# Kernel tuning notes

Hardware: AMD Instinct MI355X
Metric: run time of the kernel (lower is better)

The kernel has to match this reference:

```python
import jax, jax.numpy as jnp
import numpy as np

B, L, D, H, NB = 8, 256, 128, 4, 2
HD = D // H
N_ITEMS, TIME_SPAN = 50000, 256
EPS = 1e-8
NEG = -(2.0 ** 32) + 1.0  # torch uses -2**32+1 padding value


def _ln(x, g, b):
    m = jnp.mean(x, -1, keepdims=True)
    v = jnp.mean((x - m) ** 2, -1, keepdims=True)
    return (x - m) / jnp.sqrt(v + EPS) * g + b


def setup_inputs() -> dict:
    ks = iter(jax.random.split(jax.random.key(0), 40))

    def nrm(shape, s=0.02):
        return jax.random.normal(next(ks), shape, jnp.float32) * s

    inp = {
        "user_ids": jax.random.randint(next(ks), (B,), 0, 1000),
        "log_seqs": jax.random.randint(next(ks), (B, L), 0, N_ITEMS + 1),
        "time_matrices": jax.random.randint(next(ks), (B, L, L), 0, TIME_SPAN + 1),
        "pos_seqs": jax.random.randint(next(ks), (B, L), 1, N_ITEMS + 1),
        "neg_seqs": jax.random.randint(next(ks), (B, L), 1, N_ITEMS + 1),
    }
    inp["item_emb"] = nrm((N_ITEMS + 1, D)).at[0].set(0.0)  # padding_idx=0
    inp["posK_emb"] = nrm((L, D))
    inp["posV_emb"] = nrm((L, D))
    inp["timeK_emb"] = nrm((TIME_SPAN + 1, D))
    inp["timeV_emb"] = nrm((TIME_SPAN + 1, D))
    inp["ln1_g"] = jnp.ones((NB, D)); inp["ln1_b"] = jnp.zeros((NB, D))
    inp["Wq"] = nrm((NB, D, D)); inp["bq"] = jnp.zeros((NB, D))
    inp["Wk"] = nrm((NB, D, D)); inp["bk"] = jnp.zeros((NB, D))
    inp["Wv"] = nrm((NB, D, D)); inp["bv"] = jnp.zeros((NB, D))
    inp["ln2_g"] = jnp.ones((NB, D)); inp["ln2_b"] = jnp.zeros((NB, D))
    inp["W1"] = nrm((NB, D, D)); inp["b1"] = jnp.zeros((NB, D))
    inp["W2"] = nrm((NB, D, D)); inp["b2"] = jnp.zeros((NB, D))
    inp["lnf_g"] = jnp.ones((D,)); inp["lnf_b"] = jnp.zeros((D,))
    return inp


def reference(user_ids, log_seqs, time_matrices, pos_seqs, neg_seqs,
              item_emb, posK_emb, posV_emb, timeK_emb, timeV_emb,
              ln1_g, ln1_b, Wq, bq, Wk, bk, Wv, bv, ln2_g, ln2_b,
              W1, b1, W2, b2, lnf_g, lnf_b):
    # dropout layers are identity in eval mode
    seqs = item_emb[log_seqs] * jnp.sqrt(jnp.float32(D))          # [B,L,D]
    tK = timeK_emb[time_matrices].reshape(B, L, L, H, HD)          # [B,Lq,Lk,H,hd]
    tV = timeV_emb[time_matrices].reshape(B, L, L, H, HD)
    pad = log_seqs == 0                                            # [B,L]
    seqs = seqs * (~pad)[..., None]
    causal = jnp.triu(jnp.ones((L, L), bool), 1)                   # ~tril -> masked
    # time_mask masks by QUERY position (matches torch unsqueeze(-1).expand)
    mask = pad[:, None, :, None] | causal[None, None]              # [B,1,Lq,Lk]
    posKh = posK_emb.reshape(L, H, HD)
    posVh = posV_emb.reshape(L, H, HD)
    for i in range(NB):
        q_in = _ln(seqs, ln1_g[i], ln1_b[i])
        Qh = (q_in @ Wq[i] + bq[i]).reshape(B, L, H, HD).transpose(0, 2, 1, 3)
        Kh = (seqs @ Wk[i] + bk[i]).reshape(B, L, H, HD).transpose(0, 2, 1, 3)
        Vh = (seqs @ Wv[i] + bv[i]).reshape(B, L, H, HD).transpose(0, 2, 1, 3)
        scores = jnp.einsum("bhqd,bhkd->bhqk", Qh, Kh)
        scores = scores + jnp.einsum("bhqd,khd->bhqk", Qh, posKh)
        scores = scores + jnp.einsum("bqkhd,bhqd->bhqk", tK, Qh)
        scores = scores / jnp.sqrt(jnp.float32(HD))
        scores = jnp.where(mask, NEG, scores)
        A = jax.nn.softmax(scores, axis=-1)                        # [B,H,Lq,Lk]
        out = jnp.einsum("bhqk,bhkd->bhqd", A, Vh)
        out = out + jnp.einsum("bhqk,khd->bhqd", A, posVh)
        out = out + jnp.einsum("bhqk,bqkhd->bhqd", A, tV)
        out = out.transpose(0, 2, 1, 3).reshape(B, L, D)
        seqs = q_in + out                                          # residual on Q
        seqs = _ln(seqs, ln2_g[i], ln2_b[i])
        h = jax.nn.relu(seqs @ W1[i] + b1[i])                      # conv1d k=1 == linear
        seqs = seqs + (h @ W2[i] + b2[i])
        seqs = seqs * (~pad)[..., None]
    feats = _ln(seqs, lnf_g, lnf_b)
    pos_logits = jnp.sum(feats * item_emb[pos_seqs], -1)           # [B,L]
    neg_logits = jnp.sum(feats * item_emb[neg_seqs], -1)
    return (pos_logits, neg_logits)
```

## Files before the change

### kernel.cpp

```cpp
#include <hip/hip_runtime.h>
#include <hip/hip_bf16.h>

#define L_ 256
#define H_ 4
#define ROWS 2048
#define NEGV (-4294967295.0f)

typedef unsigned short us16;

__device__ __forceinline__ float us2f(us16 u){ return __uint_as_float(((unsigned)u)<<16); }
__device__ __forceinline__ us16 f2us(float f){ __hip_bfloat16 h=__float2bfloat16(f); return *(us16*)&h; }

__device__ __forceinline__ float dot2bf(unsigned x, unsigned y, float c){
#if __has_builtin(__builtin_amdgcn_fdot2_f32_bf16)
    typedef __bf16 bf2 __attribute__((ext_vector_type(2)));
    union U{ unsigned u; bf2 v; };
    U ux, uy; ux.u=x; uy.u=y;
    return __builtin_amdgcn_fdot2_f32_bf16(ux.v, uy.v, c, false);
#else
    float r=fmaf(us2f((us16)(x&0xffffu)), us2f((us16)(y&0xffffu)), c);
    return fmaf(us2f((us16)(x>>16)), us2f((us16)(y>>16)), r);
#endif
}

struct KArgs {
    const int *log_seqs, *tmat, *pos_seqs, *neg_seqs;
    const float *item_emb, *posK, *posV, *timeK, *timeV;
    const float *ln1g, *ln1b, *bq, *bk, *bv, *ln2g, *ln2b, *b1, *b2, *lnfg, *lnfb;
    const float *Wq, *Wk, *Wv, *W1, *W2;
    float *qin0, *qin1, *out;
    unsigned *wsP;
    us16 *tmK, *tmV, *Qb0, *Kb0, *Vb0, *Qb1, *Kb1, *Vb1;
};

struct __align__(16) Smem {
    float    sS[8*256];
    float    sPjPr[2056];
    int      sTM[512];
    unsigned sQb[128];
    float    sX[256];
    unsigned sXb[128];
    unsigned sHb[128];
    unsigned sYb[128];
    float    sRed[4], sRed2[4], sRB[8];
};

__device__ __forceinline__ float gemv128(const unsigned* __restrict__ wp,
                                         const unsigned* __restrict__ xp, int c){
    float s0=0.f, s1=0.f;
    #pragma unroll 8
    for(int kp=0;kp<64;kp+=2){
        s0=dot2bf(xp[kp],   wp[kp*128+c],     s0);
        s1=dot2bf(xp[kp+1], wp[(kp+1)*128+c], s1);
    }
    return s0+s1;
}

__device__ __forceinline__ void ln_rows(float* sA,
        const float* __restrict__ g, const float* __restrict__ b,
        float* qin_out, int r0, int tid){
    int r=tid>>5, l=tid&31;
    float* x=sA+r*128;
    float x0=x[l],x1=x[l+32],x2=x[l+64],x3=x[l+96];
    float s=x0+x1+x2+x3;
    #pragma unroll
    for(int o=16;o;o>>=1) s+=__shfl_xor(s,o,64);
    float m=s*(1.f/128.f);
    float d0=x0-m,d1=x1-m,d2=x2-m,d3=x3-m;
    float v=d0*d0+d1*d1+d2*d2+d3*d3;
    #pragma unroll
    for(int o=16;o;o>>=1) v+=__shfl_xor(v,o,64);
    float rstd=rsqrtf(v*(1.f/128.f)+1e-8f);
    float y0=d0*rstd*g[l]+b[l];
    float y1=d1*rstd*g[l+32]+b[l+32];
    float y2=d2*rstd*g[l+64]+b[l+64];
    float y3=d3*rstd*g[l+96]+b[l+96];
    x[l]=y0; x[l+32]=y1; x[l+64]=y2; x[l+96]=y3;
    if(qin_out){
        float* q=qin_out+(size_t)(r0+r)*128;
        q[l]=y0; q[l+32]=y1; q[l+64]=y2; q[l+96]=y3;
    }
}

__global__ __launch_bounds__(256) void k_pre(KArgs a){
    __shared__ __align__(16) float sA[1024];
    int tid=threadIdx.x, bid=blockIdx.x;
    if(bid<768){
        int m=bid>>8, rg=bid&255, r0=rg*8;
        {
            int rl=tid>>5, c4=tid&31;
            int id=a.log_seqs[r0+rl];
            float4 v=((const float4*)a.item_emb)[id*32+c4];
            float sc = id? 11.3137085f : 0.f;
            v.x*=sc; v.y*=sc; v.z*=sc; v.w*=sc;
            ((float4*)sA)[tid]=v;
        }
        __syncthreads();
        if(m==0){ ln_rows(sA, a.ln1g, a.ln1b, a.qin0, r0, tid); __syncthreads(); }
        const float* Wsrc=(m==0)?a.Wq:(m==1)?a.Wk:a.Wv;
        int cp=tid&63, rp=tid>>6, c0=2*cp, ra=2*rp, rb=ra+1;
        float a00=0,a01=0,a10=0,a11=0;
        const float* Ar=sA+ra*128;
        const float* Br=sA+rb*128;
        #pragma unroll 8
        for(int kk=0;kk<128;kk++){
            float2 wp=((const float2*)(Wsrc+(size_t)kk*128))[cp];
            float x0=Ar[kk], x1=Br[kk];
            a00=fmaf(x0,wp.x,a00); a01=fmaf(x0,wp.y,a01);
            a10=fmaf(x1,wp.x,a10); a11=fmaf(x1,wp.y,a11);
        }
        int r_a=r0+ra, r_b=r0+rb;
        if(m==0){
            float b0v=a.bq[c0], b1v=a.bq[c0+1];
            ushort2 s0; s0.x=f2us(a00+b0v); s0.y=f2us(a01+b1v);
            ushort2 s1; s1.x=f2us(a10+b0v); s1.y=f2us(a11+b1v);
            *(ushort2*)(a.Qb0+(size_t)r_a*128+c0)=s0;
            *(ushort2*)(a.Qb0+(size_t)r_b*128+c0)=s1;
        } else if(m==1){
            float b0v=a.bk[c0], b1v=a.bk[c0+1];
            int qa=r_a&255, qb2=r_b&255;
            ushort2 s0; s0.x=f2us(a00+b0v+a.posK[qa*128+c0]);  s0.y=f2us(a01+b1v+a.posK[qa*128+c0+1]);
            ushort2 s1; s1.x=f2us(a10+b0v+a.posK[qb2*128+c0]); s1.y=f2us(a11+b1v+a.posK[qb2*128+c0+1]);
            *(ushort2*)(a.Kb0+(size_t)r_a*128+c0)=s0;
            *(ushort2*)(a.Kb0+(size_t)r_b*128+c0)=s1;
        } else {
            float b0v=a.bv[c0], b1v=a.bv[c0+1];
            int qa=r_a&255, qb2=r_b&255;
            unsigned lo0=f2us(a00+b0v+a.posV[qa*128+c0]);
            unsigned lo1=f2us(a01+b1v+a.posV[qa*128+c0+1]);
            unsigned hi0=f2us(a10+b0v+a.posV[qb2*128+c0]);
            unsigned hi1=f2us(a11+b1v+a.posV[qb2*128+c0+1]);
            unsigned* Vo=(unsigned*)a.Vb0+((size_t)r_a>>1)*128;
            Vo[c0]  =lo0|(hi0<<16);
            Vo[c0+1]=lo1|(hi1<<16);
        }
    } else if(bid<880){
        int j=bid-768; int m=j>>4; int sub=j&15;
        const float* base;
        switch(m){
            case 0: base=a.W1; break;        case 1: base=a.W2; break;
            case 2: base=a.Wq+16384; break;  case 3: base=a.Wk+16384; break;
            case 4: base=a.Wv+16384; break;  case 5: base=a.W1+16384; break;
            default: base=a.W2+16384; break;
        }
        unsigned* dst=a.wsP+(size_t)m*8192;
        #pragma unroll
        for(int t2=0;t2<2;t2++){
            int o=sub*512+t2*256+tid;
            int kp=o>>7, c=o&127;
            unsigned lo=f2us(base[(size_t)(2*kp)*128+c]);
            unsigned hi=f2us(base[(size_t)(2*kp+1)*128+c]);
            dst[o]=lo|(hi<<16);
        }
    } else {
        int gi=(bid-880)*256+tid;
        if(gi<8224){
            float4 v=((const float4*)a.timeK)[gi];
            ushort4 o; o.x=f2us(v.x);o.y=f2us(v.y);o.z=f2us(v.z);o.w=f2us(v.w);
            ((ushort4*)a.tmK)[gi]=o;
        } else if(gi<16448){
            int g2=gi-8224;
            float4 v=((const float4*)a.timeV)[g2];
            ushort4 o; o.x=f2us(v.x);o.y=f2us(v.y);o.z=f2us(v.z);o.w=f2us(v.w);
            ((ushort4*)a.tmV)[g2]=o;
        }
    }
}

__global__ __launch_bounds__(256,7) void k_blk(KArgs a, int layer){
    __shared__ Smem sm;
    float* sPj=sm.sPjPr;
    float* sPr=sm.sPjPr;
    int tid=threadIdx.x, bid=blockIdx.x;
    int b=bid>>7, p=bid&127;
    int q1=p, q2=255-p, b0=b*L_;
    int r1=b0+q1, r2=b0+q2;
    bool pad1=a.log_seqs[r1]==0, pad2=a.log_seqs[r2]==0;
    const us16* Qb = layer? a.Qb1:a.Qb0;
    const us16* Kb = layer? a.Kb1:a.Kb0;
    const unsigned* Vbu = (const unsigned*)(layer? a.Vb1:a.Vb0);
    const float* qin = layer? a.qin1:a.qin0;
    const float scale=0.17677669529663687f;

    if(tid<128){
        int rowq=tid>>6, j=tid&63;
        int r=rowq?r2:r1;
        sm.sQb[rowq*64+j]=((const unsigned*)Qb)[(size_t)r*64+j];
    }
    sm.sTM[tid]    =a.tmat[(size_t)r1*L_+tid];
    sm.sTM[256+tid]=a.tmat[(size_t)r2*L_+tid];
    __syncthreads();

    {
        int ch=tid&15, h=ch>>2;
        uint4 qv0=((const uint4*)(sm.sQb))[ch];
        uint4 qv1=((const uint4*)(sm.sQb+64))[ch];
        for(int t=tid>>4; t<257; t+=16){
            uint4 tv=((const uint4*)(a.tmK+(size_t)t*128))[ch];
            float p0=0.f,p1=0.f;
            p0=dot2bf(qv0.x,tv.x,p0); p0=dot2bf(qv0.y,tv.y,p0);
            p0=dot2bf(qv0.z,tv.z,p0); p0=dot2bf(qv0.w,tv.w,p0);
            p1=dot2bf(qv1.x,tv.x,p1); p1=dot2bf(qv1.y,tv.y,p1);
            p1=dot2bf(qv1.z,tv.z,p1); p1=dot2bf(qv1.w,tv.w,p1);
            p0+=__shfl_xor(p0,1,64); p0+=__shfl_xor(p0,2,64);
            p1+=__shfl_xor(p1,1,64); p1+=__shfl_xor(p1,2,64);
            if((ch&3)==0){
                sPj[t*4+h]       =p0;
                sPj[1028+t*4+h]  =p1;
            }
        }
    }

    {
        int ch=tid&15, g=tid>>4, h=ch>>2;
        uint4 qv0=((const uint4*)(sm.sQb))[ch];
        uint4 qv1=((const uint4*)(sm.sQb+64))[ch];
        #pragma unroll
        for(int pass=0;pass<16;pass++){
            int k=pass*16+g;
            uint4 kv=((const uint4*)(Kb+(size_t)(b0+k)*128))[ch];
            float p0=0.f,p1=0.f;
            p0=dot2bf(qv0.x,kv.x,p0); p0=dot2bf(qv0.y,kv.y,p0);
            p0=dot2bf(qv0.z,kv.z,p0); p0=dot2bf(qv0.w,kv.w,p0);
            p1=dot2bf(qv1.x,kv.x,p1); p1=dot2bf(qv1.y,kv.y,p1);
            p1=dot2bf(qv1.z,kv.z,p1); p1=dot2bf(qv1.w,kv.w,p1);
            p0+=__shfl_xor(p0,1,64); p0+=__shfl_xor(p0,2,64);
            p1+=__shfl_xor(p1,1,64); p1+=__shfl_xor(p1,2,64);
            if((ch&3)==0){
                sm.sS[h*256+k]    =p0;
                sm.sS[(4+h)*256+k]=p1;
            }
        }
    }
    __syncthreads();

    {
        int h=tid>>6, lane=tid&63;
        #pragma unroll
        for(int i2=0;i2<2;i2++){
            int qq=i2?q2:q1; bool pad=i2?pad2:pad1;
            float* row=sm.sS+(i2*4+h)*256;
            const int*   tmr=sm.sTM+i2*256;
            const float* pjb=sPj+i2*1028;
            int k0=lane, k1=lane+64, k2=lane+128, k3=lane+192;
            float v0=(k0<=qq&&!pad)? (row[k0]+pjb[tmr[k0]*4+h])*scale : NEGV;
            float v1=(k1<=qq&&!pad)? (row[k1]+pjb[tmr[k1]*4+h])*scale : NEGV;
            float v2=(k2<=qq&&!pad)? (row[k2]+pjb[tmr[k2]*4+h])*scale : NEGV;
            float v3=(k3<=qq&&!pad)? (row[k3]+pjb[tmr[k3]*4+h])*scale : NEGV;
            float mm=fmaxf(fmaxf(v0,v1),fmaxf(v2,v3));
            #pragma unroll
            for(int o=32;o;o>>=1) mm=fmaxf(mm,__shfl_xor(mm,o,64));
            float e0=__expf(v0-mm),e1=__expf(v1-mm),e2=__expf(v2-mm),e3=__expf(v3-mm);
            float ss=e0+e1+e2+e3;
            #pragma unroll
            for(int o=32;o;o>>=1) ss+=__shfl_xor(ss,o,64);
            float inv=1.f/ss;
            us16* ar=(us16*)row;
            ar[lane]    =f2us(e0*inv); ar[lane+64] =f2us(e1*inv);
            ar[lane+128]=f2us(e2*inv); ar[lane+192]=f2us(e3*inv);
        }
    }
    __syncthreads();

    {
        int i2=tid>>7, s8=(tid>>4)&7, dq=tid&15;
        int qq=i2?q2:q1; bool pad=i2?pad2:pad1;
        int kend=pad?L_:qq+1;
        int k0=s8*32;
        int kmax=kend-k0; kmax=kmax<0?0:(kmax>32?32:kmax);
        int npair=(kmax+1)>>1;
        const unsigned* arow=(const unsigned*)(sm.sS+(i2*4+(dq>>2))*256);
        const int* tmrow=sm.sTM+i2*256;
        float ac0=0,ac1=0,ac2=0,ac3=0,ac4=0,ac5=0,ac6=0,ac7=0;
        for(int kp=0;kp<npair;kp++){
            int kx=k0+2*kp;
            unsigned aa=arow[kx>>1];
            int tma=tmrow[kx], tmb=tmrow[kx+1];
            const uint4* Vp=(const uint4*)(Vbu+((size_t)(b0+kx)>>1)*128+dq*8);
            uint4 va=Vp[0], vb4=Vp[1];
            uint4 ta=((const uint4*)(a.tmV+(size_t)tma*128))[dq];
            uint4 tb=((const uint4*)(a.tmV+(size_t)tmb*128))[dq];
            ac0=dot2bf(aa,va.x,ac0);  ac1=dot2bf(aa,va.y,ac1);
            ac2=dot2bf(aa,va.z,ac2);  ac3=dot2bf(aa,va.w,ac3);
            ac4=dot2bf(aa,vb4.x,ac4); ac5=dot2bf(aa,vb4.y,ac5);
            ac6=dot2bf(aa,vb4.z,ac6); ac7=dot2bf(aa,vb4.w,ac7);
            unsigned p0=__builtin_amdgcn_perm(tb.x,ta.x,0x05040100u);
            unsigned p1=__builtin_amdgcn_perm(tb.x,ta.x,0x07060302u);
            unsigned p2=__builtin_amdgcn_perm(tb.y,ta.y,0x05040100u);
            unsigned p3=__builtin_amdgcn_perm(tb.y,ta.y,0x07060302u);
            unsigned p4=__builtin_amdgcn_perm(tb.z,ta.z,0x05040100u);
            unsigned p5=__builtin_amdgcn_perm(tb.z,ta.z,0x07060302u);
            unsigned p6=__builtin_amdgcn_perm(tb.w,ta.w,0x05040100u);
            unsigned p7=__builtin_amdgcn_perm(tb.w,ta.w,0x07060302u);
            ac0=dot2bf(aa,p0,ac0); ac1=dot2bf(aa,p1,ac1);
            ac2=dot2bf(aa,p2,ac2); ac3=dot2bf(aa,p3,ac3);
            ac4=dot2bf(aa,p4,ac4); ac5=dot2bf(aa,p5,ac5);
            ac6=dot2bf(aa,p6,ac6); ac7=dot2bf(aa,p7,ac7);
        }
        float* dst=sPr+(i2*8+s8)*128+dq*8;
        ((float4*)dst)[0]=make_float4(ac0,ac1,ac2,ac3);
        ((float4*)dst)[1]=make_float4(ac4,ac5,ac6,ac7);
    }
    __syncthreads();

    int ii=tid>>7, l=tid&127;
    bool padown = ii? pad2:pad1;
    int rr = ii? r2:r1;
    int qown = ii? q2:q1;
    {
        float v=qin[(size_t)rr*128+l];
        #pragma unroll
        for(int sl=0;sl<8;sl++) v+=sPr[(ii*8+sl)*128+l];
        float s=v, s2=v*v;
        #pragma unroll
        for(int o=32;o;o>>=1){ s+=__shfl_xor(s,o,64); s2+=__shfl_xor(s2,o,64); }
        if((tid&63)==0){ sm.sRed[ii*2+((tid>>6)&1)]=s; sm.sRed2[ii*2+((tid>>6)&1)]=s2; }
        __syncthreads();
        float m =(sm.sRed[ii*2] +sm.sRed[ii*2+1]) *(1.f/128.f);
        float ms=(sm.sRed2[ii*2]+sm.sRed2[ii*2+1])*(1.f/128.f);
        float rstd=rsqrtf(fmaxf(ms-m*m,0.f)+1e-8f);
        float y=(v-m)*rstd*a.ln2g[layer*128+l]+a.ln2b[layer*128+l];
        sm.sX[ii*128+l]=y;
        ((us16*)sm.sXb)[ii*128+l]=f2us(y);
    }
    __syncthreads();

    int cc=l;
    {
        float h1=gemv128(a.wsP+(size_t)(layer?5:0)*8192, sm.sXb+ii*64, cc);
        h1=fmaxf(h1+a.b1[layer*128+cc],0.f);
        ((us16*)sm.sHb)[ii*128+cc]=f2us(h1);
    }
    __syncthreads();
    float f;
    {
        f=gemv128(a.wsP+(size_t)(layer?6:1)*8192, sm.sHb+ii*64, cc)
          +a.b2[layer*128+cc]+sm.sX[ii*128+cc];
        if(padown) f=0.f;
    }

    if(layer==0){
        ((us16*)sm.sYb)[ii*128+cc]=f2us(f);
        float s=f, s2=f*f;
        #pragma unroll
        for(int o=32;o;o>>=1){ s+=__shfl_xor(s,o,64); s2+=__shfl_xor(s2,o,64); }
        if((tid&63)==0){ sm.sRB[ii*2+((tid>>6)&1)]=s; sm.sRB[4+ii*2+((tid>>6)&1)]=s2; }
        __syncthreads();
        float m =(sm.sRB[ii*2]  +sm.sRB[ii*2+1]) *(1.f/128.f);
        float ms=(sm.sRB[4+ii*2]+sm.sRB[5+ii*2])*(1.f/128.f);
        float rstd=rsqrtf(fmaxf(ms-m*m,0.f)+1e-8f);
        float y1=(f-m)*rstd*a.ln1g[128+cc]+a.ln1b[128+cc];
        a.qin1[(size_t)rr*128+cc]=y1;
        ((us16*)sm.sXb)[ii*128+cc]=f2us(y1);
        __syncthreads();
        float accq=gemv128(a.wsP+(size_t)2*8192, sm.sXb+ii*64, cc)+a.bq[128+cc];
        a.Qb1[(size_t)rr*128+cc]=f2us(accq);
        float acck=gemv128(a.wsP+(size_t)3*8192, sm.sYb+ii*64, cc)+a.bk[128+cc]+a.posK[qown*128+cc];
        a.Kb1[(size_t)rr*128+cc]=f2us(acck);
        float accv=gemv128(a.wsP+(size_t)4*8192, sm.sYb+ii*64, cc)+a.bv[128+cc]+a.posV[qown*128+cc];
        ((us16*)a.Vb1)[((size_t)rr>>1)*256+2*cc+(rr&1)]=f2us(accv);
    } else {
        float s=f, s2=f*f;
        #pragma unroll
        for(int o=32;o;o>>=1){ s+=__shfl_xor(s,o,64); s2+=__shfl_xor(s2,o,64); }
        if((tid&63)==0){ sm.sRB[ii*2+((tid>>6)&1)]=s; sm.sRB[4+ii*2+((tid>>6)&1)]=s2; }
        __syncthreads();
        float m =(sm.sRB[ii*2]  +sm.sRB[ii*2+1]) *(1.f/128.f);
        float ms=(sm.sRB[4+ii*2]+sm.sRB[5+ii*2])*(1.f/128.f);
        float rstd=rsqrtf(fmaxf(ms-m*m,0.f)+1e-8f);
        sm.sX[ii*128+cc]=(f-m)*rstd*a.lnfg[cc]+a.lnfb[cc];
        __syncthreads();
        int w=tid>>6, lane=tid&63;
        int rowi=w>>1, neg=w&1;
        int rg = rowi? r2:r1;
        int id = neg? a.neg_seqs[rg] : a.pos_seqs[rg];
        const float* e=a.item_emb+(size_t)id*128;
        float s2l = sm.sX[rowi*128+lane]*e[lane] + sm.sX[rowi*128+lane+64]*e[lane+64];
        #pragma unroll
        for(int o=32;o;o>>=1) s2l+=__shfl_xor(s2l,o,64);
        if(lane==0) a.out[neg*ROWS+rg]=s2l;
    }
}

extern "C" void kernel_launch(void* const* d_in, const int* in_sizes, int n_in,
                              void* d_out, int out_size, void* d_ws, size_t ws_size,
                              hipStream_t stream) {
    KArgs a;
    a.log_seqs=(const int*)d_in[1];
    a.tmat    =(const int*)d_in[2];
    a.pos_seqs=(const int*)d_in[3];
    a.neg_seqs=(const int*)d_in[4];
    a.item_emb=(const float*)d_in[5];
    a.posK =(const float*)d_in[6];
    a.posV =(const float*)d_in[7];
    a.timeK=(const float*)d_in[8];
    a.timeV=(const float*)d_in[9];
    a.ln1g=(const float*)d_in[10];
    a.ln1b=(const float*)d_in[11];
    a.Wq=(const float*)d_in[12];
    a.bq=(const float*)d_in[13];
    a.Wk=(const float*)d_in[14];
    a.bk=(const float*)d_in[15];
    a.Wv=(const float*)d_in[16];
    a.bv=(const float*)d_in[17];
    a.ln2g=(const float*)d_in[18];
    a.ln2b=(const float*)d_in[19];
    a.W1=(const float*)d_in[20];
    a.b1=(const float*)d_in[21];
    a.W2=(const float*)d_in[22];
    a.b2=(const float*)d_in[23];
    a.lnfg=(const float*)d_in[24];
    a.lnfb=(const float*)d_in[25];

    const size_t MB=1u<<20;
    char* w=(char*)d_ws;
    a.qin0=(float*)(w+0*MB);
    a.qin1=(float*)(w+1*MB);
    a.Qb0 =(us16*) (w+2*MB);
    a.Kb0 =(us16*) (w+2*MB+512*1024);
    a.Vb0 =(us16*) (w+3*MB);
    a.Qb1 =(us16*) (w+3*MB+512*1024);
    a.Kb1 =(us16*) (w+4*MB);
    a.Vb1 =(us16*) (w+4*MB+512*1024);
    a.wsP =(unsigned*)(w+5*MB);
    a.tmK =(us16*) (w+5*MB+256*1024);
    a.tmV =(us16*) (w+5*MB+384*1024);
    a.out =(float*)d_out;

    k_pre<<<946,256,0,stream>>>(a);
    k_blk<<<1024,256,0,stream>>>(a,0);
    k_blk<<<1024,256,0,stream>>>(a,1);
}
```

Before: 192.7 us.

## Split attention and FFN/projection tail into separate kernels with 4 rows per block

The fused per-layer kernel is split in two. The attention kernel now ends after LN2 and writes its output to a new global buffer. A separate tail kernel then runs the FFN, LN and next-layer QKV projections (or the final logits), with each block handling 4 rows so every weight load from global memory feeds two rows' dot products. This halves weight traffic per row and frees shared memory in the attention kernel, at the cost of two extra launches and an extra global round-trip for the activations.

New measurement: 205.4 us. +6.6%, slower.

```diff
diff --git a/kernel.cpp b/kernel.cpp
--- a/kernel.cpp
+++ b/kernel.cpp
@@ -28,33 +28,18 @@
     const float *item_emb, *posK, *posV, *timeK, *timeV;
     const float *ln1g, *ln1b, *bq, *bk, *bv, *ln2g, *ln2b, *b1, *b2, *lnfg, *lnfb;
     const float *Wq, *Wk, *Wv, *W1, *W2;
-    float *qin0, *qin1, *out;
+    float *qin0, *qin1, *xo0, *xo1, *out;
     unsigned *wsP;
     us16 *tmK, *tmV, *Qb0, *Kb0, *Vb0, *Qb1, *Kb1, *Vb1;
 };
 
-struct __align__(16) Smem {
+struct __align__(16) SmemA {
     float    sS[8*256];
     float    sPjPr[2056];
     int      sTM[512];
     unsigned sQb[128];
-    float    sX[256];
-    unsigned sXb[128];
-    unsigned sHb[128];
-    unsigned sYb[128];
-    float    sRed[4], sRed2[4], sRB[8];
+    float    sRed[4], sRed2[4];
 };
-
-__device__ __forceinline__ float gemv128(const unsigned* __restrict__ wp,
-                                         const unsigned* __restrict__ xp, int c){
-    float s0=0.f, s1=0.f;
-    #pragma unroll 8
-    for(int kp=0;kp<64;kp+=2){
-        s0=dot2bf(xp[kp],   wp[kp*128+c],     s0);
-        s1=dot2bf(xp[kp+1], wp[(kp+1)*128+c], s1);
-    }
-    return s0+s1;
-}
 
 __device__ __forceinline__ void ln_rows(float* sA,
         const float* __restrict__ g, const float* __restrict__ b,
@@ -167,8 +152,8 @@
     }
 }
 
-__global__ __launch_bounds__(256,7) void k_blk(KArgs a, int layer){
-    __shared__ Smem sm;
+__global__ __launch_bounds__(256,7) void k_attn(KArgs a, int layer){
+    __shared__ SmemA sm;
     float* sPj=sm.sPjPr;
     float* sPr=sm.sPjPr;
     int tid=threadIdx.x, bid=blockIdx.x;
@@ -180,6 +165,7 @@
     const us16* Kb = layer? a.Kb1:a.Kb0;
     const unsigned* Vbu = (const unsigned*)(layer? a.Vb1:a.Vb0);
     const float* qin = layer? a.qin1:a.qin0;
+    float* xo = layer? a.xo1 : a.xo0;
     const float scale=0.17677669529663687f;
 
     if(tid<128){
@@ -304,9 +290,7 @@
     __syncthreads();
 
     int ii=tid>>7, l=tid&127;
-    bool padown = ii? pad2:pad1;
     int rr = ii? r2:r1;
-    int qown = ii? q2:q1;
     {
         float v=qin[(size_t)rr*128+l];
         #pragma unroll
@@ -320,65 +304,161 @@
         float ms=(sm.sRed2[ii*2]+sm.sRed2[ii*2+1])*(1.f/128.f);
         float rstd=rsqrtf(fmaxf(ms-m*m,0.f)+1e-8f);
         float y=(v-m)*rstd*a.ln2g[layer*128+l]+a.ln2b[layer*128+l];
-        sm.sX[ii*128+l]=y;
-        ((us16*)sm.sXb)[ii*128+l]=f2us(y);
+        xo[(size_t)rr*128+l]=y;
+    }
+}
+
+__global__ __launch_bounds__(256,8) void k_tail(KArgs a, int layer){
+    __shared__ __align__(16) float    xf[4*128];
+    __shared__ __align__(16) unsigned xb[4*64];
+    __shared__ __align__(16) unsigned hb[4*64];
+    __shared__ __align__(16) unsigned yb[4*64];
+    __shared__ float sR[16];
+    int tid=threadIdx.x, bid=blockIdx.x;
+    int c=tid&127, ii=tid>>7, wh=(tid>>6)&1;
+    int base=bid*4;
+    int ra=base+ii, rb=base+2+ii;
+    bool padA=a.log_seqs[ra]==0, padB=a.log_seqs[rb]==0;
+    const float* xo = layer? a.xo1 : a.xo0;
+    for(int j=tid;j<512;j+=256){
+        float v=xo[(size_t)base*128+j];
+        xf[j]=v;
+        ((us16*)xb)[j]=f2us(v);
     }
     __syncthreads();
 
-    int cc=l;
-    {
-        float h1=gemv128(a.wsP+(size_t)(layer?5:0)*8192, sm.sXb+ii*64, cc);
-        h1=fmaxf(h1+a.b1[layer*128+cc],0.f);
-        ((us16*)sm.sHb)[ii*128+cc]=f2us(h1);
+    {
+        const unsigned* wp=a.wsP+(size_t)(layer?5:0)*8192;
+        float s0=0.f,s1=0.f;
+        #pragma unroll 8
+        for(int kp=0;kp<64;kp++){
+            unsigned w=wp[kp*128+c];
+            s0=dot2bf(xb[ii*64+kp],     w, s0);
+            s1=dot2bf(xb[(ii+2)*64+kp], w, s1);
+        }
+        float b1v=a.b1[layer*128+c];
+        ((us16*)hb)[ii*128+c]    =f2us(fmaxf(s0+b1v,0.f));
+        ((us16*)hb)[(ii+2)*128+c]=f2us(fmaxf(s1+b1v,0.f));
     }
     __syncthreads();
-    float f;
-    {
-        f=gemv128(a.wsP+(size_t)(layer?6:1)*8192, sm.sHb+ii*64, cc)
-          +a.b2[layer*128+cc]+sm.sX[ii*128+cc];
-        if(padown) f=0.f;
+
+    float f0,f1;
+    {
+        const unsigned* wp=a.wsP+(size_t)(layer?6:1)*8192;
+        float s0=0.f,s1=0.f;
+        #pragma unroll 8
+        for(int kp=0;kp<64;kp++){
+            unsigned w=wp[kp*128+c];
+            s0=dot2bf(hb[ii*64+kp],     w, s0);
+            s1=dot2bf(hb[(ii+2)*64+kp], w, s1);
+        }
+        float b2v=a.b2[layer*128+c];
+        f0=s0+b2v+xf[ii*128+c];     if(padA) f0=0.f;
+        f1=s1+b2v+xf[(ii+2)*128+c]; if(padB) f1=0.f;
     }
 
     if(layer==0){
-        ((us16*)sm.sYb)[ii*128+cc]=f2us(f);
-        float s=f, s2=f*f;
-        #pragma unroll
-        for(int o=32;o;o>>=1){ s+=__shfl_xor(s,o,64); s2+=__shfl_xor(s2,o,64); }
-        if((tid&63)==0){ sm.sRB[ii*2+((tid>>6)&1)]=s; sm.sRB[4+ii*2+((tid>>6)&1)]=s2; }
+        ((us16*)yb)[ii*128+c]    =f2us(f0);
+        ((us16*)yb)[(ii+2)*128+c]=f2us(f1);
+        float s0=f0,q0=f0*f0,s1=f1,q1=f1*f1;
+        #pragma unroll
+        for(int o=32;o;o>>=1){
+            s0+=__shfl_xor(s0,o,64); q0+=__shfl_xor(q0,o,64);
+            s1+=__shfl_xor(s1,o,64); q1+=__shfl_xor(q1,o,64);
+        }
+        if((tid&63)==0){
+            sR[ii*8+wh*4+0]=s0; sR[ii*8+wh*4+1]=q0;
+            sR[ii*8+wh*4+2]=s1; sR[ii*8+wh*4+3]=q1;
+        }
         __syncthreads();
-        float m =(sm.sRB[ii*2]  +sm.sRB[ii*2+1]) *(1.f/128.f);
-        float ms=(sm.sRB[4+ii*2]+sm.sRB[5+ii*2])*(1.f/128.f);
-        float rstd=rsqrtf(fmaxf(ms-m*m,0.f)+1e-8f);
-        float y1=(f-m)*rstd*a.ln1g[128+cc]+a.ln1b[128+cc];
-        a.qin1[(size_t)rr*128+cc]=y1;
-        ((us16*)sm.sXb)[ii*128+cc]=f2us(y1);
+        float m0=(sR[ii*8+0]+sR[ii*8+4])*(1.f/128.f);
+        float e0=(sR[ii*8+1]+sR[ii*8+5])*(1.f/128.f);
+        float m1=(sR[ii*8+2]+sR[ii*8+6])*(1.f/128.f);
+        float e1=(sR[ii*8+3]+sR[ii*8+7])*(1.f/128.f);
+        float r0=rsqrtf(fmaxf(e0-m0*m0,0.f)+1e-8f);
+        float r1=rsqrtf(fmaxf(e1-m1*m1,0.f)+1e-8f);
+        float g=a.ln1g[128+c], bb=a.ln1b[128+c];
+        float y0=(f0-m0)*r0*g+bb;
+        float y1=(f1-m1)*r1*g+bb;
+        a.qin1[(size_t)ra*128+c]=y0;
+        a.qin1[(size_t)rb*128+c]=y1;
+        ((us16*)xb)[ii*128+c]    =f2us(y0);
+        ((us16*)xb)[(ii+2)*128+c]=f2us(y1);
         __syncthreads();
-        float accq=gemv128(a.wsP+(size_t)2*8192, sm.sXb+ii*64, cc)+a.bq[128+cc];
-        a.Qb1[(size_t)rr*128+cc]=f2us(accq);
-        float acck=gemv128(a.wsP+(size_t)3*8192, sm.sYb+ii*64, cc)+a.bk[128+cc]+a.posK[qown*128+cc];
-        a.Kb1[(size_t)rr*128+cc]=f2us(acck);
-        float accv=gemv128(a.wsP+(size_t)4*8192, sm.sYb+ii*64, cc)+a.bv[128+cc]+a.posV[qown*128+cc];
-        ((us16*)a.Vb1)[((size_t)rr>>1)*256+2*cc+(rr&1)]=f2us(accv);
+        {
+            const unsigned* wp=a.wsP+(size_t)2*8192;
+            float s0g=0.f,s1g=0.f;
+            #pragma unroll 8
+            for(int kp=0;kp<64;kp++){
+                unsigned w=wp[kp*128+c];
+                s0g=dot2bf(xb[ii*64+kp],     w, s0g);
+                s1g=dot2bf(xb[(ii+2)*64+kp], w, s1g);
+            }
+            float bqv=a.bq[128+c];
+            a.Qb1[(size_t)ra*128+c]=f2us(s0g+bqv);
+            a.Qb1[(size_t)rb*128+c]=f2us(s1g+bqv);
+        }
+        {
+            const unsigned* wp=a.wsP+(size_t)3*8192;
+            float s0g=0.f,s1g=0.f;
+            #pragma unroll 8
+            for(int kp=0;kp<64;kp++){
+                unsigned w=wp[kp*128+c];
+                s0g=dot2bf(yb[ii*64+kp],     w, s0g);
+                s1g=dot2bf(yb[(ii+2)*64+kp], w, s1g);
+            }
+            float bkv=a.bk[128+c];
+            a.Kb1[(size_t)ra*128+c]=f2us(s0g+bkv+a.posK[(ra&255)*128+c]);
+            a.Kb1[(size_t)rb*128+c]=f2us(s1g+bkv+a.posK[(rb&255)*128+c]);
+        }
+        {
+            const unsigned* wp=a.wsP+(size_t)4*8192;
+            float s0g=0.f,s1g=0.f;
+            #pragma unroll 8
+            for(int kp=0;kp<64;kp++){
+                unsigned w=wp[kp*128+c];
+                s0g=dot2bf(yb[ii*64+kp],     w, s0g);
+                s1g=dot2bf(yb[(ii+2)*64+kp], w, s1g);
+            }
+            float bvv=a.bv[128+c];
+            float v0=s0g+bvv+a.posV[(ra&255)*128+c];
+            float v1=s1g+bvv+a.posV[(rb&255)*128+c];
+            ((us16*)a.Vb1)[((size_t)ra>>1)*256+2*c+(ra&1)]=f2us(v0);
+            ((us16*)a.Vb1)[((size_t)rb>>1)*256+2*c+(rb&1)]=f2us(v1);
+        }
     } else {
-        float s=f, s2=f*f;
-        #pragma unroll
-        for(int o=32;o;o>>=1){ s+=__shfl_xor(s,o,64); s2+=__shfl_xor(s2,o,64); }
-        if((tid&63)==0){ sm.sRB[ii*2+((tid>>6)&1)]=s; sm.sRB[4+ii*2+((tid>>6)&1)]=s2; }
+        float s0=f0,q0=f0*f0,s1=f1,q1=f1*f1;
+        #pragma unroll
+        for(int o=32;o;o>>=1){
+            s0+=__shfl_xor(s0,o,64); q0+=__shfl_xor(q0,o,64);
+            s1+=__shfl_xor(s1,o,64); q1+=__shfl_xor(q1,o,64);
+        }
+        if((tid&63)==0){
+            sR[ii*8+wh*4+0]=s0; sR[ii*8+wh*4+1]=q0;
+            sR[ii*8+wh*4+2]=s1; sR[ii*8+wh*4+3]=q1;
+        }
         __syncthreads();
-        float m =(sm.sRB[ii*2]  +sm.sRB[ii*2+1]) *(1.f/128.f);
-        float ms=(sm.sRB[4+ii*2]+sm.sRB[5+ii*2])*(1.f/128.f);
-        float rstd=rsqrtf(fmaxf(ms-m*m,0.f)+1e-8f);
-        sm.sX[ii*128+cc]=(f-m)*rstd*a.lnfg[cc]+a.lnfb[cc];
+        float m0=(sR[ii*8+0]+sR[ii*8+4])*(1.f/128.f);
+        float e0=(sR[ii*8+1]+sR[ii*8+5])*(1.f/128.f);
+        float m1=(sR[ii*8+2]+sR[ii*8+6])*(1.f/128.f);
+        float e1=(sR[ii*8+3]+sR[ii*8+7])*(1.f/128.f);
+        float r0=rsqrtf(fmaxf(e0-m0*m0,0.f)+1e-8f);
+        float r1=rsqrtf(fmaxf(e1-m1*m1,0.f)+1e-8f);
+        float g=a.lnfg[c], bb=a.lnfb[c];
+        xf[ii*128+c]    =(f0-m0)*r0*g+bb;
+        xf[(ii+2)*128+c]=(f1-m1)*r1*g+bb;
         __syncthreads();
         int w=tid>>6, lane=tid&63;
-        int rowi=w>>1, neg=w&1;
-        int rg = rowi? r2:r1;
-        int id = neg? a.neg_seqs[rg] : a.pos_seqs[rg];
-        const float* e=a.item_emb+(size_t)id*128;
-        float s2l = sm.sX[rowi*128+lane]*e[lane] + sm.sX[rowi*128+lane+64]*e[lane+64];
-        #pragma unroll
-        for(int o=32;o;o>>=1) s2l+=__shfl_xor(s2l,o,64);
-        if(lane==0) a.out[neg*ROWS+rg]=s2l;
+        int r=base+w;
+        #pragma unroll
+        for(int neg=0;neg<2;neg++){
+            int id = neg? a.neg_seqs[r] : a.pos_seqs[r];
+            const float* e=a.item_emb+(size_t)id*128;
+            float s=xf[w*128+lane]*e[lane]+xf[w*128+lane+64]*e[lane+64];
+            #pragma unroll
+            for(int o=32;o;o>>=1) s+=__shfl_xor(s,o,64);
+            if(lane==0) a.out[neg*ROWS+r]=s;
+        }
     }
 }
 
@@ -425,9 +505,13 @@
     a.wsP =(unsigned*)(w+5*MB);
     a.tmK =(us16*) (w+5*MB+256*1024);
     a.tmV =(us16*) (w+5*MB+384*1024);
+    a.xo0 =(float*)(w+6*MB);
+    a.xo1 =(float*)(w+7*MB);
     a.out =(float*)d_out;
 
-    k_pre<<<946,256,0,stream>>>(a);
-    k_blk<<<1024,256,0,stream>>>(a,0);
-    k_blk<<<1024,256,0,stream>>>(a,1);
+    k_pre <<<946,256,0,stream>>>(a);
+    k_attn<<<1024,256,0,stream>>>(a,0);
+    k_tail<<<512,256,0,stream>>>(a,0);
+    k_attn<<<1024,256,0,stream>>>(a,1);
+    k_tail<<<512,256,0,stream>>>(a,1);
 }
```
